# Kernel optimization log

Measured on AMD Instinct MI355X. Metric: run time of the kernel, lower is better.

Reference implementation:

```python
import jax, jax.numpy as jnp
import numpy as np

B, H, SQ, SKV, D, TOPK = 1, 16, 1024, 4096, 128, 64


def setup_inputs() -> dict:
    key = jax.random.key(0)
    kq, kk, kv, ki, ks = jax.random.split(key, 5)
    q = jax.random.normal(kq, (B, H, SQ, D), dtype=jnp.float32)
    k = jax.random.normal(kk, (B, H, SKV, D), dtype=jnp.float32)
    v = jax.random.normal(kv, (B, H, SKV, D), dtype=jnp.float32)
    topk_indices = jax.random.randint(ki, (B, SQ, TOPK), 0, SKV, dtype=jnp.int32)
    topk_scores = jax.random.uniform(ks, (B, SQ, TOPK), dtype=jnp.float32)
    return {"q": q, "k": k, "v": v, "topk_indices": topk_indices,
            "topk_scores": topk_scores}


def reference(q, k, v, topk_indices, topk_scores):
    # q: (b,h,s,d); k,v: (b,h,S,d) global (cp_world_size=1 all-gather is identity)
    head_dim = q.shape[-1]
    scale = head_dim ** -0.5
    # Gather selected K/V per query without dense (b,h,s,S,d) expansion.
    # idx: (b,1,s,topk,1) broadcast against (b,h,1,S,d) along axis=3.
    idx = topk_indices[:, None, :, :, None]
    k_g = jnp.take_along_axis(k[:, :, None, :, :], idx, axis=3)  # (b,h,s,t,d)
    v_g = jnp.take_along_axis(v[:, :, None, :, :], idx, axis=3)  # (b,h,s,t,d)
    scores = jnp.einsum("bhsd,bhstd->bhst", q, k_g) * scale
    w = jax.nn.softmax(scores, axis=-1)
    # rescale by indexer scores and renormalize
    w = w * topk_scores[:, None, :, :]
    w = w / (jnp.sum(w, axis=-1, keepdims=True) + 1e-12)
    out = jnp.einsum("bhst,bhstd->bhsd", w, v_g)
    return out
```

## Files before the change

### kernel.cpp

```cpp
#include <hip/hip_runtime.h>
#include <hip/hip_fp16.h>

#define NH  16
#define SQL 1024
#define SKV 4096
#define HD  128
#define TK  64

typedef _Float16 h2_t __attribute__((ext_vector_type(2)));

__device__ __forceinline__ unsigned pkh(float x, float y) {
    return (unsigned)__half_as_ushort(__float2half(x)) |
           ((unsigned)__half_as_ushort(__float2half(y)) << 16);
}

__global__ __launch_bounds__(256) void cvt_f16(
    const float* __restrict__ k, const float* __restrict__ v,
    unsigned short* __restrict__ kh, unsigned short* __restrict__ vh)
{
    int b = blockIdx.x;
    const float* src; unsigned short* dst;
    if (b < 4096) { src = k; dst = kh; }
    else          { src = v; dst = vh; b -= 4096; }
    const size_t i = (size_t)b * 256 + threadIdx.x;
    const float4* s4 = (const float4*)src;
    float4 a = s4[2 * i], c = s4[2 * i + 1];
    uint4 o;
    o.x = pkh(a.x, a.y);
    o.y = pkh(a.z, a.w);
    o.z = pkh(c.x, c.y);
    o.w = pkh(c.z, c.w);
    ((uint4*)dst)[i] = o;
}

__global__ __launch_bounds__(256) void dsa_f16(
    const float* __restrict__ q, const unsigned short* __restrict__ kh,
    const unsigned short* __restrict__ vh, const int* __restrict__ tidx,
    const float* __restrict__ tsc, float* __restrict__ out)
{
    __shared__ float scr[4][TK][17];

    const int tid  = threadIdx.x;
    const int wv   = tid >> 6;
    const int lane = tid & 63;
    const int quad = lane >> 4;
    const int l16  = lane & 15;
    const int bi   = blockIdx.x;

    const int h = ((bi >> 11) << 3) | (bi & 7);
    const int s = (((bi >> 3) & 255) << 2) + wv;

    const float* qp = q + (size_t)(h * SQL + s) * HD + 8 * l16;
    const float4 qa = *(const float4*)qp;
    const float4 qb = *(const float4*)(qp + 4);
    h2_t q0 = {(_Float16)qa.x, (_Float16)qa.y};
    h2_t q1 = {(_Float16)qa.z, (_Float16)qa.w};
    h2_t q2 = {(_Float16)qb.x, (_Float16)qb.y};
    h2_t q3 = {(_Float16)qb.z, (_Float16)qb.w};

    const int   t_idx = tidx[s * TK + lane];
    const float t_sc  = tsc[s * TK + lane];

    const unsigned short* kb = kh + (size_t)h * SKV * HD;
    float part[16];
#pragma unroll
    for (int i = 0; i < 16; ++i) {
        const size_t row = (size_t)__shfl(t_idx, 4 * i + quad);
        uint4 kw = *(const uint4*)(kb + row * HD + 8 * l16);
        float d = 0.f;
#if __has_builtin(__builtin_amdgcn_fdot2)
        d = __builtin_amdgcn_fdot2(q0, __builtin_bit_cast(h2_t, kw.x), d, false);
        d = __builtin_amdgcn_fdot2(q1, __builtin_bit_cast(h2_t, kw.y), d, false);
        d = __builtin_amdgcn_fdot2(q2, __builtin_bit_cast(h2_t, kw.z), d, false);
        d = __builtin_amdgcn_fdot2(q3, __builtin_bit_cast(h2_t, kw.w), d, false);
#else
        {
            float2 k0 = __half22float2(__builtin_bit_cast(__half2, kw.x));
            float2 k1 = __half22float2(__builtin_bit_cast(__half2, kw.y));
            float2 k2 = __half22float2(__builtin_bit_cast(__half2, kw.z));
            float2 k3 = __half22float2(__builtin_bit_cast(__half2, kw.w));
            d  = qa.x * k0.x + qa.y * k0.y + qa.z * k1.x + qa.w * k1.y;
            d += qb.x * k2.x + qb.y * k2.y + qb.z * k3.x + qb.w * k3.y;
        }
#endif
        part[i] = d;
    }

    const unsigned short* vb = vh + (size_t)h * SKV * HD;
    uint4 vw[16];
#pragma unroll
    for (int i = 0; i < 16; ++i) {
        const size_t row = (size_t)__shfl(t_idx, 4 * i + quad);
        vw[i] = *(const uint4*)(vb + row * HD + 8 * l16);
    }

#pragma unroll
    for (int i = 0; i < 16; ++i) scr[wv][4 * i + quad][l16] = part[i];
    float acc = 0.f;
#pragma unroll
    for (int m = 0; m < 16; ++m) acc += scr[wv][lane][m];
    acc *= 0.08838834764831845f;

    float m = acc;
#pragma unroll
    for (int off = 32; off; off >>= 1) m = fmaxf(m, __shfl_xor(m, off));
    const float e   = __expf(acc - m);
    const float ets = e * t_sc;
    float se = e, sets = ets;
#pragma unroll
    for (int off = 32; off; off >>= 1) {
        se   += __shfl_xor(se, off);
        sets += __shfl_xor(sets, off);
    }
    const float w = ets / (sets + 1e-12f * se);
    const unsigned wpk = __builtin_bit_cast(unsigned, __float2half2_rn(w));

    __half2 o0 = __float2half2_rn(0.f);
    __half2 o1 = o0, o2 = o0, o3 = o0;
#pragma unroll
    for (int i = 0; i < 16; ++i) {
        const __half2 w2 = __builtin_bit_cast(__half2, __shfl(wpk, 4 * i + quad));
        o0 = __hfma2(w2, __builtin_bit_cast(__half2, vw[i].x), o0);
        o1 = __hfma2(w2, __builtin_bit_cast(__half2, vw[i].y), o1);
        o2 = __hfma2(w2, __builtin_bit_cast(__half2, vw[i].z), o2);
        o3 = __hfma2(w2, __builtin_bit_cast(__half2, vw[i].w), o3);
    }

    __half2 oo[4] = {o0, o1, o2, o3};
#pragma unroll
    for (int j = 0; j < 4; ++j) {
        unsigned u = __builtin_bit_cast(unsigned, oo[j]);
        oo[j] = __hadd2(oo[j], __builtin_bit_cast(__half2, __shfl_xor(u, 16)));
        u = __builtin_bit_cast(unsigned, oo[j]);
        oo[j] = __hadd2(oo[j], __builtin_bit_cast(__half2, __shfl_xor(u, 32)));
    }

    if (quad == 0) {
        float2 f0 = __half22float2(oo[0]);
        float2 f1 = __half22float2(oo[1]);
        float2 f2 = __half22float2(oo[2]);
        float2 f3 = __half22float2(oo[3]);
        float* op = out + (size_t)(h * SQL + s) * HD + 8 * l16;
        *(float4*)op       = make_float4(f0.x, f0.y, f1.x, f1.y);
        *(float4*)(op + 4) = make_float4(f2.x, f2.y, f3.x, f3.y);
    }
}

__global__ __launch_bounds__(256) void dsa_fp32(
    const float* __restrict__ q, const float* __restrict__ k,
    const float* __restrict__ v, const int* __restrict__ tidx,
    const float* __restrict__ tsc, float* __restrict__ out)
{
    __shared__ int   idxs[4][TK];
    __shared__ float wsc[4][TK];
    const int tid = threadIdx.x, wv = tid >> 6, lane = tid & 63;
    const int half = lane >> 5, l32 = lane & 31, bi = blockIdx.x;
    const int h = ((bi & 7) << 1) | ((bi >> 3) & 1);
    const int s = ((bi >> 4) << 2) + wv;
    const float* qp = q + (size_t)(h * SQL + s) * HD;
    const float4 qf = *(const float4*)(qp + 4 * l32);
    const float t_sc = tsc[s * TK + lane];
    idxs[wv][lane] = tidx[s * TK + lane];
    const float* kb = k + (size_t)h * SKV * HD;
#pragma unroll 4
    for (int i = 0; i < TK / 2; ++i) {
        const int t = 2 * i + half, row = idxs[wv][t];
        float4 k4 = *(const float4*)(kb + (size_t)row * HD + 4 * l32);
        float d = k4.x * qf.x + k4.y * qf.y + k4.z * qf.z + k4.w * qf.w;
        d += __shfl_xor(d, 16); d += __shfl_xor(d, 8); d += __shfl_xor(d, 4);
        d += __shfl_xor(d, 2);  d += __shfl_xor(d, 1);
        if (l32 == 0) wsc[wv][t] = d;
    }
    float acc = wsc[wv][lane] * 0.08838834764831845f;
    float m = acc;
#pragma unroll
    for (int off = 32; off; off >>= 1) m = fmaxf(m, __shfl_xor(m, off));
    const float e = __expf(acc - m), ets = e * t_sc;
    float se = e, sets = ets;
#pragma unroll
    for (int off = 32; off; off >>= 1) { se += __shfl_xor(se, off); sets += __shfl_xor(sets, off); }
    wsc[wv][lane] = ets / (sets + 1e-12f * se);
    const float* vbp = v + (size_t)h * SKV * HD;
    float4 o = make_float4(0.f, 0.f, 0.f, 0.f);
#pragma unroll 4
    for (int i = 0; i < TK / 2; ++i) {
        const int t = 2 * i + half, row = idxs[wv][t];
        const float wt = wsc[wv][t];
        float4 v4 = *(const float4*)(vbp + (size_t)row * HD + 4 * l32);
        o.x += wt * v4.x; o.y += wt * v4.y; o.z += wt * v4.z; o.w += wt * v4.w;
    }
    o.x += __shfl_xor(o.x, 32); o.y += __shfl_xor(o.y, 32);
    o.z += __shfl_xor(o.z, 32); o.w += __shfl_xor(o.w, 32);
    if (half == 0) *(float4*)(out + (size_t)(h * SQL + s) * HD + 4 * l32) = o;
}

extern "C" void kernel_launch(void* const* d_in, const int* in_sizes, int n_in,
                              void* d_out, int out_size, void* d_ws, size_t ws_size,
                              hipStream_t stream) {
    const float* q  = (const float*)d_in[0];
    const float* k  = (const float*)d_in[1];
    const float* v  = (const float*)d_in[2];
    const int*   ti = (const int*)d_in[3];
    const float* ts = (const float*)d_in[4];
    float* out = (float*)d_out;

    const size_t nkv  = (size_t)NH * SKV * HD;
    const size_t need = 2 * nkv * sizeof(unsigned short);
    if (ws_size >= need) {
        unsigned short* kh = (unsigned short*)d_ws;
        unsigned short* vh = kh + nkv;
        cvt_f16<<<dim3(8192), dim3(256), 0, stream>>>(k, v, kh, vh);
        dsa_f16<<<dim3(4096), dim3(256), 0, stream>>>(q, kh, vh, ti, ts, out);
    } else {
        dsa_fp32<<<dim3(4096), dim3(256), 0, stream>>>(q, k, v, ti, ts, out);
    }
}
```

Before: 134.1 us.

## Split fused sparse attention into separate QK-softmax and PV kernels

Breaks the single fused kernel into two launches. The first computes QK scores and normalized softmax weights and writes them to a workspace stash. The second reloads the weights and gathers V rows to accumulate the output. This cuts per-kernel register pressure by dropping the 16 held V vectors, which may raise occupancy. The cost is an extra launch, an extra global round trip for the weights, and the loss of V-load prefetching overlapped with the QK compute.

```diff
diff --git a/kernel.cpp b/kernel.cpp
--- a/kernel.cpp
+++ b/kernel.cpp
@@ -33,10 +33,10 @@
     ((uint4*)dst)[i] = o;
 }
 
-__global__ __launch_bounds__(256) void dsa_f16(
+__global__ __launch_bounds__(256) void qk_f16(
     const float* __restrict__ q, const unsigned short* __restrict__ kh,
-    const unsigned short* __restrict__ vh, const int* __restrict__ tidx,
-    const float* __restrict__ tsc, float* __restrict__ out)
+    const int* __restrict__ tidx, const float* __restrict__ tsc,
+    float* __restrict__ wstash)
 {
     __shared__ float scr[4][TK][17];
 
@@ -86,14 +86,6 @@
         part[i] = d;
     }
 
-    const unsigned short* vb = vh + (size_t)h * SKV * HD;
-    uint4 vw[16];
-#pragma unroll
-    for (int i = 0; i < 16; ++i) {
-        const size_t row = (size_t)__shfl(t_idx, 4 * i + quad);
-        vw[i] = *(const uint4*)(vb + row * HD + 8 * l16);
-    }
-
 #pragma unroll
     for (int i = 0; i < 16; ++i) scr[wv][4 * i + quad][l16] = part[i];
     float acc = 0.f;
@@ -112,18 +104,40 @@
         se   += __shfl_xor(se, off);
         sets += __shfl_xor(sets, off);
     }
-    const float w = ets / (sets + 1e-12f * se);
+    wstash[(size_t)(h * SQL + s) * TK + lane] = ets / (sets + 1e-12f * se);
+}
+
+__global__ __launch_bounds__(256) void pv_f16(
+    const unsigned short* __restrict__ vh, const int* __restrict__ tidx,
+    const float* __restrict__ wstash, float* __restrict__ out)
+{
+    const int tid  = threadIdx.x;
+    const int wv   = tid >> 6;
+    const int lane = tid & 63;
+    const int quad = lane >> 4;
+    const int l16  = lane & 15;
+    const int bi   = blockIdx.x;
+
+    const int h = ((bi >> 11) << 3) | (bi & 7);
+    const int s = (((bi >> 3) & 255) << 2) + wv;
+
+    const int   t_idx = tidx[s * TK + lane];
+    const float w     = wstash[(size_t)(h * SQL + s) * TK + lane];
     const unsigned wpk = __builtin_bit_cast(unsigned, __float2half2_rn(w));
 
+    const unsigned short* vb = vh + (size_t)h * SKV * HD;
     __half2 o0 = __float2half2_rn(0.f);
     __half2 o1 = o0, o2 = o0, o3 = o0;
 #pragma unroll
     for (int i = 0; i < 16; ++i) {
-        const __half2 w2 = __builtin_bit_cast(__half2, __shfl(wpk, 4 * i + quad));
-        o0 = __hfma2(w2, __builtin_bit_cast(__half2, vw[i].x), o0);
-        o1 = __hfma2(w2, __builtin_bit_cast(__half2, vw[i].y), o1);
-        o2 = __hfma2(w2, __builtin_bit_cast(__half2, vw[i].z), o2);
-        o3 = __hfma2(w2, __builtin_bit_cast(__half2, vw[i].w), o3);
+        const int src = 4 * i + quad;
+        const size_t row = (size_t)__shfl(t_idx, src);
+        const __half2 w2 = __builtin_bit_cast(__half2, __shfl(wpk, src));
+        uint4 vw = *(const uint4*)(vb + row * HD + 8 * l16);
+        o0 = __hfma2(w2, __builtin_bit_cast(__half2, vw.x), o0);
+        o1 = __hfma2(w2, __builtin_bit_cast(__half2, vw.y), o1);
+        o2 = __hfma2(w2, __builtin_bit_cast(__half2, vw.z), o2);
+        o3 = __hfma2(w2, __builtin_bit_cast(__half2, vw.w), o3);
     }
 
     __half2 oo[4] = {o0, o1, o2, o3};
@@ -204,13 +218,17 @@
     const float* ts = (const float*)d_in[4];
     float* out = (float*)d_out;
 
-    const size_t nkv  = (size_t)NH * SKV * HD;
-    const size_t need = 2 * nkv * sizeof(unsigned short);
+    const size_t nkv   = (size_t)NH * SKV * HD;
+    const size_t wneed = (size_t)NH * SQL * TK;
+    const size_t need  = 2 * nkv * sizeof(unsigned short)
+                       + wneed * sizeof(float);
     if (ws_size >= need) {
         unsigned short* kh = (unsigned short*)d_ws;
         unsigned short* vh = kh + nkv;
+        float* wstash = (float*)(vh + nkv);
         cvt_f16<<<dim3(8192), dim3(256), 0, stream>>>(k, v, kh, vh);
-        dsa_f16<<<dim3(4096), dim3(256), 0, stream>>>(q, kh, vh, ti, ts, out);
+        qk_f16<<<dim3(4096), dim3(256), 0, stream>>>(q, kh, ti, ts, wstash);
+        pv_f16<<<dim3(4096), dim3(256), 0, stream>>>(vh, ti, wstash, out);
     } else {
         dsa_fp32<<<dim3(4096), dim3(256), 0, stream>>>(q, k, v, ti, ts, out);
     }
```

After: 135.8 us. Within noise of the previous version (+1.3%).
